# Optimization experiments

Measured on AMD Instinct MI355X. Metric: run time of the kernel, lower is better.

## Reference

```python
import jax, jax.numpy as jnp
import numpy as np

S1, S2, B, H, E, IN, OUT, NL = 8, 32, 256, 1024, 512, 2, 2, 4


def setup_inputs() -> dict:
    key = jax.random.key(0)
    ks = jax.random.split(key, 20)
    s_h = 1.0 / np.sqrt(H)
    inp = {
        'input': jax.random.normal(ks[0], (B, IN), jnp.float32),
        'h0': jax.random.normal(ks[1], (NL, B, H), jnp.float32) * 0.5,
        'c0': jax.random.normal(ks[2], (NL, B, H), jnp.float32) * 0.5,
        'all_outputs': jax.random.normal(ks[3], (S1, S2, B, H), jnp.float32),
        'W_emb': jax.random.normal(ks[4], (E, IN), jnp.float32) / np.sqrt(IN),
        'b_emb': jax.random.normal(ks[5], (E,), jnp.float32) * 0.01,
        'W_attn': jax.random.normal(ks[6], (1, 2 * H), jnp.float32) / np.sqrt(2 * H),
        'b_attn': jax.random.normal(ks[7], (1,), jnp.float32) * 0.01,
        'Wih0': jax.random.normal(ks[8], (4 * H, E + H), jnp.float32) / np.sqrt(E + H),
        'Whh0': jax.random.normal(ks[9], (4 * H, H), jnp.float32) * s_h,
        'bih0': jax.random.normal(ks[10], (4 * H,), jnp.float32) * 0.01,
        'bhh0': jax.random.normal(ks[11], (4 * H,), jnp.float32) * 0.01,
        'Wih_r': jax.random.normal(ks[12], (NL - 1, 4 * H, H), jnp.float32) * s_h,
        'Whh_r': jax.random.normal(ks[13], (NL - 1, 4 * H, H), jnp.float32) * s_h,
        'bih_r': jax.random.normal(ks[14], (NL - 1, 4 * H), jnp.float32) * 0.01,
        'bhh_r': jax.random.normal(ks[15], (NL - 1, 4 * H), jnp.float32) * 0.01,
        'W_out': jax.random.normal(ks[16], (OUT, H), jnp.float32) * s_h,
        'b_out': jax.random.normal(ks[17], (OUT,), jnp.float32) * 0.01,
    }
    return inp


def _lstm_cell(x, h, c, Wih, Whh, bih, bhh):
    g = x @ Wih.T + h @ Whh.T + bih + bhh  # [B, 4H], torch gate order i,f,g,o
    i, f, gg, o = jnp.split(g, 4, axis=1)
    c2 = jax.nn.sigmoid(f) * c + jax.nn.sigmoid(i) * jnp.tanh(gg)
    h2 = jax.nn.sigmoid(o) * jnp.tanh(c2)
    return h2, c2


def reference(input, h0, c0, all_outputs, W_emb, b_emb, W_attn, b_attn,
              Wih0, Whh0, bih0, bhh0, Wih_r, Whh_r, bih_r, bhh_r, W_out, b_out):
    s1, s2, b, h_dim = all_outputs.shape
    # embedding (dropout = identity in eval mode)
    embedded = jax.nn.relu(input @ W_emb.T + b_emb)  # [B, E]
    h_top = h0[0]  # [B, H]
    # attn(cat(h_top, y)) decomposed: h part is shared across all (j, i)
    w_h = W_attn[0, :h_dim]
    w_y = W_attn[0, h_dim:]
    scores = (jnp.einsum('jibh,h->jib', all_outputs, w_y)
              + (h_top @ w_h)[None, None, :] + b_attn[0])  # [S1, S2, B]
    # torch cats per-(j,i) [B,1] columns j-major -> [B, S1*S2]
    normalized = jax.nn.softmax(scores.reshape(s1 * s2, b).T, axis=1)  # [B, S1*S2]
    temp = normalized.reshape(b, s1, s2)
    # NOTE: original writes into an expand()-ed zero buffer, so every j-slice
    # aliases the same memory; after the loop all slices equal the last j's bmm
    # result and sum(0) multiplies it by S1. We replicate that exactly.
    applied_last = jnp.einsum('bi,ibh->bh', temp[:, -1, :], all_outputs[-1])  # [B, H]
    final_attn = s1 * applied_last
    x = jnp.concatenate([final_attn, embedded], axis=1)  # [B, H+E]
    hs, cs = [], []
    h, c = _lstm_cell(x, h0[0], c0[0], Wih0, Whh0, bih0, bhh0)
    hs.append(h); cs.append(c)
    for l in range(Wih_r.shape[0]):  # inter-layer dropout = identity in eval
        h, c = _lstm_cell(h, h0[l + 1], c0[l + 1], Wih_r[l], Whh_r[l], bih_r[l], bhh_r[l])
        hs.append(h); cs.append(c)
    h_new = jnp.stack(hs)
    c_new = jnp.stack(cs)
    final_output = h @ W_out.T + b_out  # [B, OUT]
    return final_output, h_new, c_new, normalized
```

## Files before the change

### kernel.cpp

```cpp
#include <hip/hip_runtime.h>
#include <hip/hip_bf16.h>

typedef __bf16 bf16x8 __attribute__((ext_vector_type(8)));
typedef float  f32x4  __attribute__((ext_vector_type(4)));

#define O_FINAL 0
#define O_H     512
#define O_C     1049088
#define O_NORM  2097664

__device__ __forceinline__ bf16x8 cvt8(float4 a, float4 b) {
  bf16x8 r;
  r[0] = (__bf16)a.x; r[1] = (__bf16)a.y; r[2] = (__bf16)a.z; r[3] = (__bf16)a.w;
  r[4] = (__bf16)b.x; r[5] = (__bf16)b.y; r[6] = (__bf16)b.z; r[7] = (__bf16)b.w;
  return r;
}

template<int K>
__device__ __forceinline__ void tile_gemm_ff(const float* __restrict__ A,
                                             const float* __restrict__ W,
                                             int r0, int j0, char* lds,
                                             f32x4 acc[2]) {
  constexpr int NK = K / 64;
  constexpr int D = 4;
  const int t = threadIdx.x, lane = t & 63, wave = t >> 6;
  const int rf = wave & 3, gg = wave >> 2;
  const int tr = t >> 3, chunk = t & 7;
  const float* wsrc = W + (size_t)((tr >> 4) * 1024 + j0 + (tr & 15)) * K + chunk * 8;
  const float* asrc = A + (size_t)(r0 + tr) * K + chunk * 8;
  const int sw_off = (chunk ^ (tr & 7)) << 4;
  const int woff = 8192 + tr * 128 + sw_off;
  const int aoff = tr * 128 + sw_off;
  const int a_tr  = rf * 16 + (lane & 15);
  const int w_tr0 = gg * 32 + (lane & 15);
  const int w_tr1 = w_tr0 + 16;
  const int ksel  = lane >> 4;

  float4 wp[D][2], ap[D][2];
#pragma unroll
  for (int d = 0; d < D; ++d) {
    wp[d][0] = *(const float4*)(wsrc + d * 64);
    wp[d][1] = *(const float4*)(wsrc + d * 64 + 4);
    ap[d][0] = *(const float4*)(asrc + d * 64);
    ap[d][1] = *(const float4*)(asrc + d * 64 + 4);
  }
#pragma unroll
  for (int s = 0; s < NK; ++s) {
    const int sl = s % D;
    char* buf = lds + (s & 1) * 16384;
    *(bf16x8*)(buf + aoff) = cvt8(ap[sl][0], ap[sl][1]);
    *(bf16x8*)(buf + woff) = cvt8(wp[sl][0], wp[sl][1]);
    if (s + D < NK) {
      wp[sl][0] = *(const float4*)(wsrc + (s + D) * 64);
      wp[sl][1] = *(const float4*)(wsrc + (s + D) * 64 + 4);
      ap[sl][0] = *(const float4*)(asrc + (s + D) * 64);
      ap[sl][1] = *(const float4*)(asrc + (s + D) * 64 + 4);
    }
    __syncthreads();
#pragma unroll
    for (int s2 = 0; s2 < 2; ++s2) {
      const int chk = s2 * 4 + ksel;
      bf16x8 af  = *(const bf16x8*)(buf + a_tr * 128 + ((chk ^ (a_tr & 7)) << 4));
      bf16x8 wf0 = *(const bf16x8*)(buf + 8192 + w_tr0 * 128 + ((chk ^ (w_tr0 & 7)) << 4));
      bf16x8 wf1 = *(const bf16x8*)(buf + 8192 + w_tr1 * 128 + ((chk ^ (w_tr1 & 7)) << 4));
      acc[0] = __builtin_amdgcn_mfma_f32_16x16x32_bf16(af, wf0, acc[0], 0, 0, 0);
      acc[1] = __builtin_amdgcn_mfma_f32_16x16x32_bf16(af, wf1, acc[1], 0, 0, 0);
    }
  }
}

__global__ __launch_bounds__(512) void k_front(
    const float* __restrict__ AO, const float* __restrict__ Wattn,
    float* __restrict__ sc,
    const float* __restrict__ h0,
    const float* __restrict__ Whh0, const float* __restrict__ Whh_r,
    const float* __restrict__ bih0, const float* __restrict__ bhh0,
    const float* __restrict__ bih_r, const float* __restrict__ bhh_r,
    float* __restrict__ Gh) {
  const int t = threadIdx.x, lane = t & 63, wave = t >> 6;
  if (blockIdx.x < 2048) {
    const float* wy = Wattn + 1024;
    float4 wv[4];
#pragma unroll
    for (int q = 0; q < 4; ++q) wv[q] = *(const float4*)(wy + lane * 4 + 256 * q);
    const int row0 = (blockIdx.x * 8 + wave) * 4;
    float a4[4];
#pragma unroll
    for (int rr = 0; rr < 4; ++rr) {
      const float4* rp = (const float4*)(AO + (size_t)(row0 + rr) * 1024);
      float a = 0.f;
#pragma unroll
      for (int q = 0; q < 4; ++q) {
        float4 v = rp[lane + 64 * q];
        a += v.x * wv[q].x + v.y * wv[q].y + v.z * wv[q].z + v.w * wv[q].w;
      }
      a4[rr] = a;
    }
#pragma unroll
    for (int rr = 0; rr < 4; ++rr) {
      float a = a4[rr];
#pragma unroll
      for (int off = 32; off; off >>= 1) a += __shfl_xor(a, off, 64);
      if (lane == 0) {
        int row = row0 + rr;
        sc[(row & 255) * 256 + (row >> 8)] = a;
      }
    }
    return;
  }
  __shared__ char smem[32768];
  const int j = blockIdx.x - 2048;
  const int l = j >> 8, inner = j & 255;
  const int cb = inner & 63, rb = inner >> 6;
  const int j0 = cb * 16, r0 = rb * 64;
  const float* A  = h0 + (size_t)l * 262144;
  const float* W  = (l == 0) ? Whh0 : (Whh_r + (size_t)(l - 1) * 4194304);
  const float* bi = (l == 0) ? bih0 : (bih_r + (size_t)(l - 1) * 4096);
  const float* bh = (l == 0) ? bhh0 : (bhh_r + (size_t)(l - 1) * 4096);
  f32x4 acc[2] = {};
  tile_gemm_ff<1024>(A, W, r0, j0, smem, acc);
  float* Go = Gh + (size_t)l * 1048576;
  const int rf = wave & 3, gg = wave >> 2;
  const int col = j0 + (lane & 15);
  const int rbase = r0 + rf * 16 + ((lane >> 4) << 2);
#pragma unroll
  for (int gi = 0; gi < 2; ++gi) {
    const int cg = (gg * 2 + gi) * 1024 + col;
#pragma unroll
    for (int q = 0; q < 4; ++q)
      Go[(size_t)(rbase + q) * 4096 + cg] = acc[gi][q] + bi[cg] + bh[cg];
  }
}

__global__ __launch_bounds__(256) void k_smx(const float* __restrict__ sc,
                                             const float* __restrict__ AO,
                                             const float* __restrict__ inp,
                                             const float* __restrict__ Wemb,
                                             const float* __restrict__ bemb,
                                             float* __restrict__ norm_out,
                                             __bf16* __restrict__ x) {
  __shared__ float red[4];
  __shared__ float wsm[32];
  const int b = blockIdx.x, t = threadIdx.x, lane = t & 63, wave = t >> 6;
  float s = sc[b * 256 + t];
  float m = s;
#pragma unroll
  for (int off = 32; off; off >>= 1) m = fmaxf(m, __shfl_xor(m, off, 64));
  if (lane == 0) red[wave] = m;
  __syncthreads();
  m = fmaxf(fmaxf(red[0], red[1]), fmaxf(red[2], red[3]));
  float e = __expf(s - m);
  float sum = e;
#pragma unroll
  for (int off = 32; off; off >>= 1) sum += __shfl_xor(sum, off, 64);
  __syncthreads();
  if (lane == 0) red[wave] = sum;
  __syncthreads();
  sum = red[0] + red[1] + red[2] + red[3];
  float nv = e / sum;
  norm_out[b * 256 + t] = nv;
  if (t >= 224) wsm[t - 224] = nv;
  __syncthreads();
  float acc[4] = {0.f, 0.f, 0.f, 0.f};
  const float* base = AO + ((size_t)224 * 256 + b) * 1024;
#pragma unroll 4
  for (int i = 0; i < 32; ++i) {
    float w = wsm[i];
    const float* rp = base + (size_t)i * 262144;
#pragma unroll
    for (int q = 0; q < 4; ++q) acc[q] += w * rp[t + 256 * q];
  }
#pragma unroll
  for (int q = 0; q < 4; ++q) x[(size_t)b * 1536 + t + 256 * q] = (__bf16)(8.0f * acc[q]);
  float i0 = inp[b * 2], i1 = inp[b * 2 + 1];
#pragma unroll
  for (int r = 0; r < 2; ++r) {
    int jj = t + 256 * r;
    float e2 = i0 * Wemb[jj * 2] + i1 * Wemb[jj * 2 + 1] + bemb[jj];
    x[(size_t)b * 1536 + 1024 + jj] = (__bf16)fmaxf(e2, 0.f);
  }
}

template<int KA>
__global__ __launch_bounds__(512) void k_layer(const __bf16* __restrict__ A,
                                               const float* __restrict__ Wih,
                                               const float* __restrict__ Gh,
                                               const float* __restrict__ c0l,
                                               float* __restrict__ h_out,
                                               float* __restrict__ c_out,
                                               __bf16* __restrict__ hb) {
  constexpr int NK = KA / 64;
  constexpr int D = 4;
  __shared__ char smem[30720];
  float* exch = (float*)(smem + 24576);
  const int t = threadIdx.x, lane = t & 63, wave = t >> 6;
  const int rf = wave & 1, g = wave >> 1;
  const int cb = blockIdx.x & 63, rb = blockIdx.x >> 6;
  const int j0 = cb * 16, r0 = rb * 32;
  const int tr = t >> 3, chunk = t & 7;
  const float* wsrc = Wih + (size_t)((tr >> 4) * 1024 + j0 + (tr & 15)) * KA + chunk * 8;
  const int woff = 4096 + tr * 128 + ((chunk ^ (tr & 7)) << 4);
  const __bf16* asrc = A + (size_t)(r0 + (t >> 3)) * KA + chunk * 8;
  const int aoff = (t >> 3) * 128 + ((chunk ^ ((t >> 3) & 7)) << 4);
  const bool do_a = (t < 256);
  const int a_tr = rf * 16 + (lane & 15);
  const int w_tr = g * 16 + (lane & 15);
  const int ksel = lane >> 4;

  float4 wp[D][2]; bf16x8 ap[D];
#pragma unroll
  for (int d = 0; d < D; ++d) {
    wp[d][0] = *(const float4*)(wsrc + d * 64);
    wp[d][1] = *(const float4*)(wsrc + d * 64 + 4);
    if (do_a) ap[d] = *(const bf16x8*)(asrc + d * 64);
  }
  f32x4 acc = {0.f, 0.f, 0.f, 0.f};
#pragma unroll
  for (int s = 0; s < NK; ++s) {
    const int sl = s % D;
    char* buf = smem + (s & 1) * 12288;
    if (do_a) *(bf16x8*)(buf + aoff) = ap[sl];
    *(bf16x8*)(buf + woff) = cvt8(wp[sl][0], wp[sl][1]);
    if (s + D < NK) {
      wp[sl][0] = *(const float4*)(wsrc + (s + D) * 64);
      wp[sl][1] = *(const float4*)(wsrc + (s + D) * 64 + 4);
      if (do_a) ap[sl] = *(const bf16x8*)(asrc + (s + D) * 64);
    }
    __syncthreads();
#pragma unroll
    for (int s2 = 0; s2 < 2; ++s2) {
      const int chk = s2 * 4 + ksel;
      bf16x8 af = *(const bf16x8*)(buf + a_tr * 128 + ((chk ^ (a_tr & 7)) << 4));
      bf16x8 wf = *(const bf16x8*)(buf + 4096 + w_tr * 128 + ((chk ^ (w_tr & 7)) << 4));
      acc = __builtin_amdgcn_mfma_f32_16x16x32_bf16(af, wf, acc, 0, 0, 0);
    }
  }
  const int col = j0 + (lane & 15);
  const int rbase = r0 + rf * 16 + ((lane >> 4) << 2);
  const int eidx = ((lane >> 4) << 2) * 16 + (lane & 15);
#pragma unroll
  for (int q = 0; q < 4; ++q)
    acc[q] += Gh[(size_t)(rbase + q) * 4096 + g * 1024 + col];
  __syncthreads();
  if (g > 0) {
#pragma unroll
    for (int q = 0; q < 4; ++q)
      exch[((g - 1) * 2 + rf) * 256 + eidx + q * 16] = acc[q];
  }
  __syncthreads();
  if (g == 0) {
#pragma unroll
    for (int q = 0; q < 4; ++q) {
      const int row = rbase + q;
      float gf = exch[(0 * 2 + rf) * 256 + eidx + q * 16];
      float gv = exch[(1 * 2 + rf) * 256 + eidx + q * 16];
      float go = exch[(2 * 2 + rf) * 256 + eidx + q * 16];
      float si = 1.f / (1.f + __expf(-acc[q]));
      float sf = 1.f / (1.f + __expf(-gf));
      float so = 1.f / (1.f + __expf(-go));
      float c2 = sf * c0l[(size_t)row * 1024 + col] + si * tanhf(gv);
      float h2 = so * tanhf(c2);
      h_out[(size_t)row * 1024 + col] = h2;
      c_out[(size_t)row * 1024 + col] = c2;
      hb[(size_t)row * 1024 + col] = (__bf16)h2;
    }
  }
}

__global__ __launch_bounds__(256) void k_final(const float* __restrict__ h3,
                                               const float* __restrict__ Wout,
                                               const float* __restrict__ bout,
                                               float* __restrict__ out) {
  const int lane = threadIdx.x & 63, wave = threadIdx.x >> 6;
  const int b = blockIdx.x * 4 + wave;
  const float4* hp = (const float4*)(h3 + (size_t)b * 1024);
  const float4* w0 = (const float4*)Wout;
  const float4* w1 = (const float4*)(Wout + 1024);
  float a0 = 0.f, a1 = 0.f;
#pragma unroll
  for (int q = 0; q < 4; ++q) {
    float4 hv = hp[lane + 64 * q];
    float4 v0 = w0[lane + 64 * q];
    float4 v1 = w1[lane + 64 * q];
    a0 += hv.x * v0.x + hv.y * v0.y + hv.z * v0.z + hv.w * v0.w;
    a1 += hv.x * v1.x + hv.y * v1.y + hv.z * v1.z + hv.w * v1.w;
  }
#pragma unroll
  for (int off = 32; off; off >>= 1) {
    a0 += __shfl_xor(a0, off, 64);
    a1 += __shfl_xor(a1, off, 64);
  }
  if (lane == 0) {
    out[b * 2]     = a0 + bout[0];
    out[b * 2 + 1] = a1 + bout[1];
  }
}

extern "C" void kernel_launch(void* const* d_in, const int* in_sizes, int n_in,
                              void* d_out, int out_size, void* d_ws, size_t ws_size,
                              hipStream_t stream) {
  const float* inp    = (const float*)d_in[0];
  const float* h0     = (const float*)d_in[1];
  const float* c0     = (const float*)d_in[2];
  const float* AO     = (const float*)d_in[3];
  const float* Wemb   = (const float*)d_in[4];
  const float* bemb   = (const float*)d_in[5];
  const float* Wattn  = (const float*)d_in[6];
  const float* Wih0   = (const float*)d_in[8];
  const float* Whh0   = (const float*)d_in[9];
  const float* bih0   = (const float*)d_in[10];
  const float* bhh0   = (const float*)d_in[11];
  const float* Wih_r  = (const float*)d_in[12];
  const float* Whh_r  = (const float*)d_in[13];
  const float* bih_r  = (const float*)d_in[14];
  const float* bhh_r  = (const float*)d_in[15];
  const float* Wout   = (const float*)d_in[16];
  const float* bout   = (const float*)d_in[17];

  float* out = (float*)d_out;
  char* ws = (char*)d_ws;

  float*  sc = (float*)ws;
  float*  Gh = (float*)(ws + 262144);
  __bf16* xb = (__bf16*)(ws + 17039360);
  __bf16* hb = (__bf16*)(ws + 17825792);

  k_front<<<3072, 512, 0, stream>>>(AO, Wattn, sc, h0, Whh0, Whh_r,
                                    bih0, bhh0, bih_r, bhh_r, Gh);
  k_smx<<<256, 256, 0, stream>>>(sc, AO, inp, Wemb, bemb, out + O_NORM, xb);

  k_layer<1536><<<512, 512, 0, stream>>>(xb, Wih0, Gh, c0,
                                         out + O_H, out + O_C, hb);
  for (int l = 1; l < 4; ++l)
    k_layer<1024><<<512, 512, 0, stream>>>(hb + (size_t)(l - 1) * 262144,
                                           Wih_r + (size_t)(l - 1) * 4194304,
                                           Gh + (size_t)l * 1048576,
                                           c0 + (size_t)l * 262144,
                                           out + O_H + (size_t)l * 262144,
                                           out + O_C + (size_t)l * 262144,
                                           hb + (size_t)l * 262144);

  k_final<<<64, 256, 0, stream>>>(out + O_H + 3 * 262144, Wout, bout, out + O_FINAL);
}
```

Measured before the change: 164.6 us.

## Retile LSTM layer kernel so each block covers all batch rows and four columns

```diff
diff --git a/kernel.cpp b/kernel.cpp
--- a/kernel.cpp
+++ b/kernel.cpp
@@ -191,78 +191,96 @@
                                                __bf16* __restrict__ hb) {
   constexpr int NK = KA / 64;
   constexpr int D = 4;
-  __shared__ char smem[30720];
-  float* exch = (float*)(smem + 24576);
+  __shared__ char smem[69632];
   const int t = threadIdx.x, lane = t & 63, wave = t >> 6;
-  const int rf = wave & 1, g = wave >> 1;
-  const int cb = blockIdx.x & 63, rb = blockIdx.x >> 6;
-  const int j0 = cb * 16, r0 = rb * 32;
-  const int tr = t >> 3, chunk = t & 7;
-  const float* wsrc = Wih + (size_t)((tr >> 4) * 1024 + j0 + (tr & 15)) * KA + chunk * 8;
-  const int woff = 4096 + tr * 128 + ((chunk ^ (tr & 7)) << 4);
-  const __bf16* asrc = A + (size_t)(r0 + (t >> 3)) * KA + chunk * 8;
-  const int aoff = (t >> 3) * 128 + ((chunk ^ ((t >> 3) & 7)) << 4);
-  const bool do_a = (t < 256);
-  const int a_tr = rf * 16 + (lane & 15);
-  const int w_tr = g * 16 + (lane & 15);
-  const int ksel = lane >> 4;
-
-  float4 wp[D][2]; bf16x8 ap[D];
+  const int j0 = blockIdx.x * 4;
+  const int atr = t >> 1, ahalf = t & 1;
+  const __bf16* asrc = A + (size_t)atr * KA + ahalf * 32;
+  const int wr = t >> 3, wch = t & 7;
+  const float* wsrc = Wih + (size_t)((wr >> 2) * 1024 + j0 + (wr & 3)) * KA + wch * 8;
+  const bool do_w = (t < 128);
+  const int a_trb = wave * 32 + (lane & 15);
+  const int w_tr  = lane & 15;
+  const int ksel  = lane >> 4;
+
+  bf16x8 ap[D][4]; float4 wp[D][2];
 #pragma unroll
   for (int d = 0; d < D; ++d) {
-    wp[d][0] = *(const float4*)(wsrc + d * 64);
-    wp[d][1] = *(const float4*)(wsrc + d * 64 + 4);
-    if (do_a) ap[d] = *(const bf16x8*)(asrc + d * 64);
-  }
-  f32x4 acc = {0.f, 0.f, 0.f, 0.f};
+#pragma unroll
+    for (int c = 0; c < 4; ++c) ap[d][c] = *(const bf16x8*)(asrc + d * 64 + c * 8);
+    if (do_w) {
+      wp[d][0] = *(const float4*)(wsrc + d * 64);
+      wp[d][1] = *(const float4*)(wsrc + d * 64 + 4);
+    }
+  }
+  f32x4 acc[2] = {};
 #pragma unroll
   for (int s = 0; s < NK; ++s) {
     const int sl = s % D;
-    char* buf = smem + (s & 1) * 12288;
-    if (do_a) *(bf16x8*)(buf + aoff) = ap[sl];
-    *(bf16x8*)(buf + woff) = cvt8(wp[sl][0], wp[sl][1]);
+    char* abuf = smem + (s & 1) * 32768;
+    char* wbuf = smem + 65536 + (s & 1) * 2048;
+#pragma unroll
+    for (int c = 0; c < 4; ++c) {
+      const int chunk = ahalf * 4 + c;
+      *(bf16x8*)(abuf + atr * 128 + ((chunk ^ (atr & 7)) << 4)) = ap[sl][c];
+    }
+    if (do_w)
+      *(bf16x8*)(wbuf + wr * 128 + ((wch ^ (wr & 7)) << 4)) = cvt8(wp[sl][0], wp[sl][1]);
     if (s + D < NK) {
-      wp[sl][0] = *(const float4*)(wsrc + (s + D) * 64);
-      wp[sl][1] = *(const float4*)(wsrc + (s + D) * 64 + 4);
-      if (do_a) ap[sl] = *(const bf16x8*)(asrc + (s + D) * 64);
+#pragma unroll
+      for (int c = 0; c < 4; ++c)
+        ap[sl][c] = *(const bf16x8*)(asrc + (s + D) * 64 + c * 8);
+      if (do_w) {
+        wp[sl][0] = *(const float4*)(wsrc + (s + D) * 64);
+        wp[sl][1] = *(const float4*)(wsrc + (s + D) * 64 + 4);
+      }
     }
     __syncthreads();
 #pragma unroll
     for (int s2 = 0; s2 < 2; ++s2) {
       const int chk = s2 * 4 + ksel;
-      bf16x8 af = *(const bf16x8*)(buf + a_tr * 128 + ((chk ^ (a_tr & 7)) << 4));
-      bf16x8 wf = *(const bf16x8*)(buf + 4096 + w_tr * 128 + ((chk ^ (w_tr & 7)) << 4));
-      acc = __builtin_amdgcn_mfma_f32_16x16x32_bf16(af, wf, acc, 0, 0, 0);
-    }
-  }
-  const int col = j0 + (lane & 15);
-  const int rbase = r0 + rf * 16 + ((lane >> 4) << 2);
-  const int eidx = ((lane >> 4) << 2) * 16 + (lane & 15);
-#pragma unroll
-  for (int q = 0; q < 4; ++q)
-    acc[q] += Gh[(size_t)(rbase + q) * 4096 + g * 1024 + col];
-  __syncthreads();
-  if (g > 0) {
+      bf16x8 wf = *(const bf16x8*)(wbuf + w_tr * 128 + ((chk ^ (w_tr & 7)) << 4));
+#pragma unroll
+      for (int rf = 0; rf < 2; ++rf) {
+        const int a_tr = a_trb + rf * 16;
+        bf16x8 af = *(const bf16x8*)(abuf + a_tr * 128 + ((chk ^ (a_tr & 7)) << 4));
+        acc[rf] = __builtin_amdgcn_mfma_f32_16x16x32_bf16(af, wf, acc[rf], 0, 0, 0);
+      }
+    }
+  }
+  const int col = j0 + (lane & 3);
+  const int gi = (lane >> 2) & 3;
+#pragma unroll
+  for (int rf = 0; rf < 2; ++rf) {
+    const int rbase = wave * 32 + rf * 16 + ((lane >> 4) << 2);
 #pragma unroll
     for (int q = 0; q < 4; ++q)
-      exch[((g - 1) * 2 + rf) * 256 + eidx + q * 16] = acc[q];
-  }
-  __syncthreads();
-  if (g == 0) {
+      acc[rf][q] += Gh[(size_t)(rbase + q) * 4096 + gi * 1024 + col];
+  }
+#pragma unroll
+  for (int rf = 0; rf < 2; ++rf) {
+    const int rbase = wave * 32 + rf * 16 + ((lane >> 4) << 2);
+    float v4[4], v8[4], v12[4];
 #pragma unroll
     for (int q = 0; q < 4; ++q) {
-      const int row = rbase + q;
-      float gf = exch[(0 * 2 + rf) * 256 + eidx + q * 16];
-      float gv = exch[(1 * 2 + rf) * 256 + eidx + q * 16];
-      float go = exch[(2 * 2 + rf) * 256 + eidx + q * 16];
-      float si = 1.f / (1.f + __expf(-acc[q]));
-      float sf = 1.f / (1.f + __expf(-gf));
-      float so = 1.f / (1.f + __expf(-go));
-      float c2 = sf * c0l[(size_t)row * 1024 + col] + si * tanhf(gv);
-      float h2 = so * tanhf(c2);
-      h_out[(size_t)row * 1024 + col] = h2;
-      c_out[(size_t)row * 1024 + col] = c2;
-      hb[(size_t)row * 1024 + col] = (__bf16)h2;
+      v4[q]  = __shfl_xor(acc[rf][q], 4, 64);
+      v8[q]  = __shfl_xor(acc[rf][q], 8, 64);
+      v12[q] = __shfl_xor(acc[rf][q], 12, 64);
+    }
+    if (gi == 0) {
+#pragma unroll
+      for (int q = 0; q < 4; ++q) {
+        const int row = rbase + q;
+        float si = 1.f / (1.f + __expf(-acc[rf][q]));
+        float sf = 1.f / (1.f + __expf(-v4[q]));
+        float gv = tanhf(v8[q]);
+        float so = 1.f / (1.f + __expf(-v12[q]));
+        float c2 = sf * c0l[(size_t)row * 1024 + col] + si * gv;
+        float h2 = so * tanhf(c2);
+        h_out[(size_t)row * 1024 + col] = h2;
+        c_out[(size_t)row * 1024 + col] = c2;
+        hb[(size_t)row * 1024 + col] = (__bf16)h2;
+      }
     }
   }
 }
@@ -329,10 +347,10 @@
                                     bih0, bhh0, bih_r, bhh_r, Gh);
   k_smx<<<256, 256, 0, stream>>>(sc, AO, inp, Wemb, bemb, out + O_NORM, xb);
 
-  k_layer<1536><<<512, 512, 0, stream>>>(xb, Wih0, Gh, c0,
+  k_layer<1536><<<256, 512, 0, stream>>>(xb, Wih0, Gh, c0,
                                          out + O_H, out + O_C, hb);
   for (int l = 1; l < 4; ++l)
-    k_layer<1024><<<512, 512, 0, stream>>>(hb + (size_t)(l - 1) * 262144,
+    k_layer<1024><<<256, 512, 0, stream>>>(hb + (size_t)(l - 1) * 262144,
                                            Wih_r + (size_t)(l - 1) * 4194304,
                                            Gh + (size_t)l * 1048576,
                                            c0 + (size_t)l * 262144,
```

Result: slower. 201.3 us (+22.3%).
